# Optimization experiments

Hardware: AMD Instinct MI355X
Metric: run time of the kernel (lower is better)

The kernel has to match this reference:

```python
import jax, jax.numpy as jnp
import numpy as np
from jax.scipy.ndimage import map_coordinates

# module hyperparameters (match init_kwargs)
N = 64          # patch size
GRIDSIZE = 2
C = GRIDSIZE * GRIDSIZE   # channels = patches per solution region
PADDED = 192    # padded canvas size
B = 512


def setup_inputs() -> dict:
    key = jax.random.key(0)
    k1, k2 = jax.random.split(key)
    patches = jax.random.normal(k1, (B, N, N, C), dtype=jnp.float32)
    # sub-pixel scan offsets (dx, dy); keep translated patch inside the canvas
    max_off = (PADDED - N) / 2.0 - 1.0
    positions = jax.random.uniform(k2, (B, 1, 2, C), dtype=jnp.float32,
                                   minval=-max_off, maxval=max_off)
    return {"patches": patches, "positions": positions}


def _translate_one(img, txy):
    # img: (P, P); txy = (dx, dy). tfa.image.translate semantics:
    # out(y, x) = img(y - dy, x - dx), bilinear interpolation, zero fill.
    P = img.shape[0]
    grid = jnp.arange(P, dtype=img.dtype)
    rows = jnp.broadcast_to(grid[:, None] - txy[1], (P, P))
    cols = jnp.broadcast_to(grid[None, :] - txy[0], (P, P))
    return map_coordinates(img, [rows, cols], order=1, mode='constant', cval=0.0)


def reference(patches, positions):
    Bv, Nv, _, Cv = patches.shape
    pad_lo = (PADDED - Nv) // 2
    pad_hi = PADDED - Nv - pad_lo
    # center-pad each NxN patch into the padded canvas
    padded = jnp.pad(patches, ((0, 0), (pad_lo, pad_hi), (pad_lo, pad_hi), (0, 0)))
    # channel -> flat: (B*C, P, P)
    imgs = padded.transpose(0, 3, 1, 2).reshape(Bv * Cv, PADDED, PADDED)
    # (B,1,2,C) -> (B*C, 2) as (dx, dy)
    offs = positions[:, 0].transpose(0, 2, 1).reshape(Bv * Cv, 2)
    translated = jax.vmap(_translate_one)(imgs, offs)
    # sum translated patches over the channel axis -> (B, P, P, 1)
    out = translated.reshape(Bv, Cv, PADDED, PADDED).sum(axis=1)[..., None]
    return out
```

## Files before the change

### kernel.cpp

```cpp
#include <hip/hip_runtime.h>

#define PATCH_N 64
#define CH      4
#define PADDED  192
#define BATCH   512
#define THREADS 1024
#define PROWS   66
#define PCOLS   76
#define PLANE_F (PROWS * PCOLS)
#define LDS_F   (CH * PLANE_F)

__device__ __forceinline__ int   rfl_i(int x)   { return __builtin_amdgcn_readfirstlane(x); }
__device__ __forceinline__ float rfl_f(float x) { return __int_as_float(__builtin_amdgcn_readfirstlane(__float_as_int(x))); }

__global__ __launch_bounds__(THREADS, 8)
void reassemble_h(const float* __restrict__ patches,
                  const float* __restrict__ positions,
                  float* __restrict__ out)
{
    __shared__ float4 lds4[LDS_F / 4];
    float* __restrict__ lds = reinterpret_cast<float*>(lds4);

    const int b    = blockIdx.x;
    const int tid  = threadIdx.x;
    const int lane = tid & 63;
    const int wid  = rfl_i(tid >> 6);

    const float* pos = positions + (size_t)b * 8;
    int   syc[CH], ac[CH], padc[CH];
    float wx0c[CH], wx1c[CH], wy0c[CH], wy1c[CH];
#pragma unroll
    for (int c = 0; c < CH; ++c) {
        const float tx  = 64.f + rfl_f(pos[c]);
        const float sxf = ceilf(tx);
        const int   sx  = rfl_i((int)sxf);
        wx1c[c] = rfl_f(sxf - tx);
        wx0c[c] = 1.f - wx1c[c];
        const float ty  = 64.f + rfl_f(pos[CH + c]);
        const float syf = ceilf(ty);
        syc[c]  = rfl_i((int)syf);
        wy1c[c] = rfl_f(syf - ty);
        wy0c[c] = 1.f - wy1c[c];
        ac[c]   = (sx - 1) >> 2;
        padc[c] = (sx - 1) & 3;
    }

#pragma unroll
    for (int j = 0; j < (LDS_F / 4 + THREADS - 1) / THREADS; ++j) {
        const int idx = j * THREADS + tid;
        if (idx < LDS_F / 4) lds4[idx] = make_float4(0.f, 0.f, 0.f, 0.f);
    }
    __syncthreads();

    const float4* __restrict__ p4 =
        reinterpret_cast<const float4*>(patches) + (size_t)b * (PATCH_N * PATCH_N);
    const bool last = (lane == 63);
#pragma unroll
    for (int pass = 0; pass < 4; ++pass) {
        const int r = pass * 16 + wid;
        const float4 v = p4[r * PATCH_N + lane];
#pragma unroll
        for (int c = 0; c < CH; ++c) {
            const float val = (c == 0) ? v.x : (c == 1) ? v.y : (c == 2) ? v.z : v.w;
            float vr = __shfl_down(val, 1);
            vr = last ? 0.f : vr;
            const float h = fmaf(wx1c[c], vr, wx0c[c] * val);
            float* pl = lds + c * PLANE_F + (r + 1) * PCOLS;
            pl[lane + padc[c] + 5] = h;
            if (lane == 0) pl[padc[c] + 4] = wx1c[c] * val;
        }
    }
    __syncthreads();

    float4* __restrict__ o4 =
        reinterpret_cast<float4*>(out) + (size_t)b * (PADDED * PADDED / 4);

#pragma unroll
    for (int it = 0; it < (PADDED * PADDED / 4) / THREADS; ++it) {
        const int idx = it * THREADS + tid;
        const int y   = idx / 48;
        const int xg  = idx - y * 48;
        const int y0  = rfl_i(y);
        const int yp1 = y + 1;
        float a0 = 0.f, a1 = 0.f, a2 = 0.f, a3 = 0.f;

#pragma unroll
        for (int c = 0; c < CH; ++c) {
            if (y0 + 2 < syc[c] - 1 || y0 > syc[c] + 63) continue;

            const int t    = yp1 - syc[c];
            const int row0 = min(max(t, 0), 65);
            const int row1 = min(max(t, -1), 64) + 1;
            const int q4   = min(max(xg - ac[c] + 1, 0), 18);
            const int base = c * (PLANE_F / 4) + q4;
            const float4 W0 = lds4[base + row0 * (PCOLS / 4)];
            const float4 W1 = lds4[base + row1 * (PCOLS / 4)];

            const float wy0 = wy0c[c], wy1 = wy1c[c];
            a0 = fmaf(wy0, W0.x, a0); a0 = fmaf(wy1, W1.x, a0);
            a1 = fmaf(wy0, W0.y, a1); a1 = fmaf(wy1, W1.y, a1);
            a2 = fmaf(wy0, W0.z, a2); a2 = fmaf(wy1, W1.z, a2);
            a3 = fmaf(wy0, W0.w, a3); a3 = fmaf(wy1, W1.w, a3);
        }

        o4[idx] = make_float4(a0, a1, a2, a3);
    }
}

extern "C" void kernel_launch(void* const* d_in, const int* in_sizes, int n_in,
                              void* d_out, int out_size, void* d_ws, size_t ws_size,
                              hipStream_t stream) {
    const float* patches   = (const float*)d_in[0];
    const float* positions = (const float*)d_in[1];
    float* out = (float*)d_out;

    reassemble_h<<<dim3(BATCH), THREADS, 0, stream>>>(patches, positions, out);
}
```

Measured before the change: 99.98 us.

## Zero only LDS borders and compute two output rows per thread

LDS initialization now zeros only the padding rows and columns that the horizontal pass does not write, so the full-buffer clear and its barrier are removed. The output loop gives each thread two vertically adjacent rows, sharing the middle LDS row load (3 loads instead of 4 for two outputs). This cuts LDS traffic and the zeroing stores, but raises register pressure and leaves half the threads idle in the last iteration.

Result: no change. 100.5 us (+0.5%).

```diff
diff --git a/kernel.cpp b/kernel.cpp
--- a/kernel.cpp
+++ b/kernel.cpp
@@ -8,6 +8,7 @@
 #define PROWS   66
 #define PCOLS   76
 #define PLANE_F (PROWS * PCOLS)
+#define PLANE4  (PLANE_F / 4)
 #define LDS_F   (CH * PLANE_F)
 
 __device__ __forceinline__ int   rfl_i(int x)   { return __builtin_amdgcn_readfirstlane(x); }
@@ -45,12 +46,24 @@
         padc[c] = (sx - 1) & 3;
     }
 
+    if (tid < 152) {
+        const int c   = tid / 38;
+        const int s   = tid % 38;
+        const int row = (s < 19) ? 0 : 65;
+        const int g   = (s < 19) ? s : s - 19;
+        lds4[c * PLANE4 + row * (PCOLS / 4) + g] = make_float4(0.f, 0.f, 0.f, 0.f);
+    }
 #pragma unroll
-    for (int j = 0; j < (LDS_F / 4 + THREADS - 1) / THREADS; ++j) {
-        const int idx = j * THREADS + tid;
-        if (idx < LDS_F / 4) lds4[idx] = make_float4(0.f, 0.f, 0.f, 0.f);
+    for (int j = 0; j < 4; ++j) {
+        const int s   = j * THREADS + tid;
+        const int c   = s >> 10;
+        const int r   = 1 + ((s >> 4) & 63);
+        const int k   = s & 15;
+        const int col = (k < 8) ? k : (60 + k);
+        const bool z  = (k < 8) ? (col < padc[c] + 4)
+                                : (col >= padc[c] + 69);
+        if (z) lds[c * PLANE_F + r * PCOLS + col] = 0.f;
     }
-    __syncthreads();
 
     const float4* __restrict__ p4 =
         reinterpret_cast<const float4*>(patches) + (size_t)b * (PATCH_N * PATCH_N);
@@ -76,34 +89,44 @@
         reinterpret_cast<float4*>(out) + (size_t)b * (PADDED * PADDED / 4);
 
 #pragma unroll
-    for (int it = 0; it < (PADDED * PADDED / 4) / THREADS; ++it) {
-        const int idx = it * THREADS + tid;
-        const int y   = idx / 48;
-        const int xg  = idx - y * 48;
-        const int y0  = rfl_i(y);
-        const int yp1 = y + 1;
+    for (int it = 0; it < 5; ++it) {
+        if (it == 4 && tid >= 512) continue;
+        const int task = it * THREADS + tid;
+        const int pr   = task / 48;
+        const int xg   = task - pr * 48;
+        const int y    = pr * 2;
+        const int y0   = rfl_i(y);
         float a0 = 0.f, a1 = 0.f, a2 = 0.f, a3 = 0.f;
+        float b0 = 0.f, b1 = 0.f, b2 = 0.f, b3 = 0.f;
 
 #pragma unroll
         for (int c = 0; c < CH; ++c) {
-            if (y0 + 2 < syc[c] - 1 || y0 > syc[c] + 63) continue;
+            if (y0 + 5 < syc[c] - 1 || y0 > syc[c] + 63) continue;
 
-            const int t    = yp1 - syc[c];
-            const int row0 = min(max(t, 0), 65);
-            const int row1 = min(max(t, -1), 64) + 1;
-            const int q4   = min(max(xg - ac[c] + 1, 0), 18);
-            const int base = c * (PLANE_F / 4) + q4;
-            const float4 W0 = lds4[base + row0 * (PCOLS / 4)];
-            const float4 W1 = lds4[base + row1 * (PCOLS / 4)];
+            const int t  = y + 1 - syc[c];
+            const int r0 = min(max(t,     0), 65);
+            const int r1 = min(max(t + 1, 0), 65);
+            const int r2 = min(max(t + 2, 0), 65);
+            const int q4 = min(max(xg - ac[c] + 1, 0), 18);
+            const int base = c * PLANE4 + q4;
+            const float4 W0 = lds4[base + r0 * (PCOLS / 4)];
+            const float4 W1 = lds4[base + r1 * (PCOLS / 4)];
+            const float4 W2 = lds4[base + r2 * (PCOLS / 4)];
 
             const float wy0 = wy0c[c], wy1 = wy1c[c];
             a0 = fmaf(wy0, W0.x, a0); a0 = fmaf(wy1, W1.x, a0);
             a1 = fmaf(wy0, W0.y, a1); a1 = fmaf(wy1, W1.y, a1);
             a2 = fmaf(wy0, W0.z, a2); a2 = fmaf(wy1, W1.z, a2);
             a3 = fmaf(wy0, W0.w, a3); a3 = fmaf(wy1, W1.w, a3);
+            b0 = fmaf(wy0, W1.x, b0); b0 = fmaf(wy1, W2.x, b0);
+            b1 = fmaf(wy0, W1.y, b1); b1 = fmaf(wy1, W2.y, b1);
+            b2 = fmaf(wy0, W1.z, b2); b2 = fmaf(wy1, W2.z, b2);
+            b3 = fmaf(wy0, W1.w, b3); b3 = fmaf(wy1, W2.w, b3);
         }
 
-        o4[idx] = make_float4(a0, a1, a2, a3);
+        const int idx0 = y * 48 + xg;
+        o4[idx0]      = make_float4(a0, a1, a2, a3);
+        o4[idx0 + 48] = make_float4(b0, b1, b2, b3);
     }
 }
 
```
